# Performance work log

Hardware: AMD Instinct MI355X
Metric: run time of the kernel (lower is better)

Reference implementation:

```python
import jax, jax.numpy as jnp
import numpy as np

N_GRAPHS = 500
EPS = 1e-5


def setup_inputs() -> dict:
    key = jax.random.key(0)
    ks = jax.random.split(key, 10)
    N, H, OUT, E = 50000, 96, 10, 800000
    s = 1.0 / np.sqrt(H)
    x = jax.random.normal(ks[0], (N, H), jnp.float32)
    edge_index = jax.random.randint(ks[1], (2, E), 0, N, jnp.int32)
    batch = jnp.sort(jax.random.randint(ks[2], (N,), 0, N_GRAPHS, jnp.int32))
    convW = jax.random.normal(ks[3], (6, H, H), jnp.float32) * s
    convB = jnp.zeros((6, H), jnp.float32)
    bnG = jnp.ones((5, H), jnp.float32)
    bnB = jnp.zeros((5, H), jnp.float32)
    W1 = jax.random.normal(ks[4], (H, H), jnp.float32) * s
    b1 = jnp.zeros((H,), jnp.float32)
    g1 = jnp.ones((H,), jnp.float32)
    be1 = jnp.zeros((H,), jnp.float32)
    W2 = jax.random.normal(ks[5], (H, H), jnp.float32) * s
    b2 = jnp.zeros((H,), jnp.float32)
    W3 = jax.random.normal(ks[6], (H, OUT), jnp.float32) * s
    b3 = jnp.zeros((OUT,), jnp.float32)
    return dict(x=x, edge_index=edge_index, batch=batch, convW=convW, convB=convB,
                bnG=bnG, bnB=bnB, W1=W1, b1=b1, g1=g1, be1=be1, W2=W2, b2=b2, W3=W3, b3=b3)


def _batchnorm(h, g, b):
    # track_running_stats=False -> always use batch statistics (biased var)
    mu = h.mean(axis=0)
    v = jnp.mean((h - mu) ** 2, axis=0)
    return (h - mu) * jax.lax.rsqrt(v + EPS) * g + b


def reference(x, edge_index, batch, convW, convB, bnG, bnB, W1, b1, g1, be1, W2, b2, W3, b3):
    N = x.shape[0]
    src, dst = edge_index[0], edge_index[1]
    # GCN symmetric normalization with self-loops: A_hat = D^-1/2 (A+I) D^-1/2
    deg = jnp.zeros((N,), x.dtype).at[dst].add(1.0) + 1.0  # +1 for self loop
    dinv = jax.lax.rsqrt(deg)
    ew = dinv[src] * dinv[dst]            # [E] edge weights
    self_w = dinv * dinv                   # [N] self-loop weights (1/deg)

    def gcn_conv(h, W, b):
        h = h @ W
        agg = jnp.zeros_like(h).at[dst].add(ew[:, None] * h[src])
        return agg + self_w[:, None] * h + b

    # PyG BasicGNN: layers 0..4 -> conv+norm+relu+dropout; layer 5 -> conv only.
    # Dropout is identity in eval mode.
    for i in range(6):
        x = gcn_conv(x, convW[i], convB[i])
        if i < 5:
            x = jax.nn.relu(_batchnorm(x, bnG[i], bnB[i]))

    # global_mean_pool over `batch`
    cnt = jax.ops.segment_sum(jnp.ones((N,), x.dtype), batch, num_segments=N_GRAPHS)
    pooled = jax.ops.segment_sum(x, batch, num_segments=N_GRAPHS) / jnp.maximum(cnt, 1.0)[:, None]

    # prediction head: Linear -> BN -> ReLU -> (Dropout) -> Linear -> ReLU -> Linear
    h = jax.nn.relu(_batchnorm(pooled @ W1 + b1, g1, be1))
    h = jax.nn.relu(h @ W2 + b2)
    return h @ W3 + b3
```

## Files before the change

kernel.cpp:

```cpp
#include <hip/hip_runtime.h>
#include <hip/hip_fp16.h>

#define HF 96
#define C4 24
#define CH 12
#define NGRAPHS 500
#define EPS 1e-5f

__device__ __forceinline__ float4 h4tof4(uint2 u) {
    __half2 a = *(__half2*)&u.x;
    __half2 b = *(__half2*)&u.y;
    float2 fa = __half22float2(a);
    float2 fb = __half22float2(b);
    return make_float4(fa.x, fa.y, fb.x, fb.y);
}


__global__ void count_kernel(const int* __restrict__ dst, int E, int* __restrict__ cnt) {
    int stride = gridDim.x * blockDim.x;
    for (int i = blockIdx.x * blockDim.x + threadIdx.x; i < E; i += stride)
        atomicAdd(&cnt[dst[i]], 1);
}

__global__ void node_init_kernel(const int* __restrict__ cnt, int N,
                                 float* __restrict__ dinv, float* __restrict__ selfw) {
    int stride = gridDim.x * blockDim.x;
    for (int i = blockIdx.x * blockDim.x + threadIdx.x; i < N; i += stride) {
        float d = (float)(cnt[i] + 1);
        dinv[i] = 1.0f / sqrtf(d);
        selfw[i] = 1.0f / d;
    }
}

__global__ void scan1_kernel(const int* __restrict__ cnt, int N, int* __restrict__ bsum) {
    __shared__ int s[256];
    int t = threadIdx.x;
    int i = blockIdx.x * 256 + t;
    s[t] = (i < N) ? cnt[i] : 0;
    __syncthreads();
    for (int off = 128; off; off >>= 1) {
        if (t < off) s[t] += s[t + off];
        __syncthreads();
    }
    if (t == 0) bsum[blockIdx.x] = s[0];
}

__global__ void scan2_kernel(const int* __restrict__ bsum, int NB,
                             int* __restrict__ boff, int* __restrict__ row_ptr, int N) {
    __shared__ int s[256];
    int t = threadIdx.x;
    int v = (t < NB) ? bsum[t] : 0;
    s[t] = v;
    __syncthreads();
    for (int off = 1; off < 256; off <<= 1) {
        int u = (t >= off) ? s[t - off] : 0;
        __syncthreads();
        s[t] += u;
        __syncthreads();
    }
    if (t < NB) boff[t] = s[t] - v;
    if (t == 255) row_ptr[N] = s[255];
}

__global__ void scan3_kernel(int* __restrict__ cnt, int N, const int* __restrict__ boff,
                             int* __restrict__ row_ptr) {
    __shared__ int s[256];
    int t = threadIdx.x;
    int i = blockIdx.x * 256 + t;
    int v = (i < N) ? cnt[i] : 0;
    s[t] = v;
    __syncthreads();
    for (int off = 1; off < 256; off <<= 1) {
        int u = (t >= off) ? s[t - off] : 0;
        __syncthreads();
        s[t] += u;
        __syncthreads();
    }
    if (i < N) {
        row_ptr[i] = boff[blockIdx.x] + s[t] - v;
        cnt[i] = 0;
    }
}

__global__ void scatter_kernel(const int* __restrict__ src, const int* __restrict__ dst, int E,
                               const int* __restrict__ row_ptr, int* __restrict__ cnt,
                               const float* __restrict__ dinv,
                               int2* __restrict__ csr) {
    int stride = gridDim.x * blockDim.x;
    for (int i = blockIdx.x * blockDim.x + threadIdx.x; i < E; i += stride) {
        int d = dst[i], s = src[i];
        int p = row_ptr[d] + atomicAdd(&cnt[d], 1);
        float w = dinv[s] * dinv[d];
        csr[p] = make_int2(s, __float_as_int(w));
    }
}


__global__ __launch_bounds__(256) void
matmul_kernel(const float* __restrict__ in, const float* __restrict__ W,
              __half* __restrict__ out, int N, int applyBN,
              const double* __restrict__ bnsum,
              const float* __restrict__ bnG, const float* __restrict__ bnB) {
    __shared__ float4 sW[HF * C4];
    __shared__ float4 sAl[C4], sBe[C4];
    for (int i = threadIdx.x; i < HF * C4; i += blockDim.x)
        sW[i] = ((const float4*)W)[i];
    if (threadIdx.x < HF) {
        float a = 1.f, b = 0.f;
        if (applyBN) {
            double invN = 1.0 / (double)N;
            double mu = bnsum[threadIdx.x] * invN;
            double var = bnsum[HF + threadIdx.x] * invN - mu * mu;
            float v = fmaxf((float)var, 0.f) + EPS;
            a = bnG[threadIdx.x] / sqrtf(v);
            b = bnB[threadIdx.x] - (float)mu * a;
        }
        ((float*)sAl)[threadIdx.x] = a;
        ((float*)sBe)[threadIdx.x] = b;
    }
    __syncthreads();
    int nG = (N + 3) >> 2;
    int total = nG * C4;
    int stride = gridDim.x * blockDim.x;
    for (int idx = blockIdx.x * blockDim.x + threadIdx.x; idx < total; idx += stride) {
        int ng = idx / C4, c = idx % C4;
        int n0 = ng * 4;
        int rem = N - n0;
        const float4* r0 = (const float4*)(in + (size_t)n0 * HF);
        const float4* r1 = r0 + ((rem > 1) ? C4 : 0);
        const float4* r2 = r0 + ((rem > 2) ? 2 * C4 : 0);
        const float4* r3 = r0 + ((rem > 3) ? 3 * C4 : 0);
        float4 acc0 = make_float4(0.f, 0.f, 0.f, 0.f);
        float4 acc1 = acc0, acc2 = acc0, acc3 = acc0;
#pragma unroll 4
        for (int k4 = 0; k4 < C4; ++k4) {
            float4 al = sAl[k4], be = sBe[k4];
            float4 w0 = sW[(k4 * 4 + 0) * C4 + c];
            float4 w1 = sW[(k4 * 4 + 1) * C4 + c];
            float4 w2 = sW[(k4 * 4 + 2) * C4 + c];
            float4 w3 = sW[(k4 * 4 + 3) * C4 + c];
            float4 a0 = r0[k4], a1 = r1[k4], a2 = r2[k4], a3 = r3[k4];
            if (applyBN) {
                a0.x = fmaxf(fmaf(a0.x, al.x, be.x), 0.f); a0.y = fmaxf(fmaf(a0.y, al.y, be.y), 0.f);
                a0.z = fmaxf(fmaf(a0.z, al.z, be.z), 0.f); a0.w = fmaxf(fmaf(a0.w, al.w, be.w), 0.f);
                a1.x = fmaxf(fmaf(a1.x, al.x, be.x), 0.f); a1.y = fmaxf(fmaf(a1.y, al.y, be.y), 0.f);
                a1.z = fmaxf(fmaf(a1.z, al.z, be.z), 0.f); a1.w = fmaxf(fmaf(a1.w, al.w, be.w), 0.f);
                a2.x = fmaxf(fmaf(a2.x, al.x, be.x), 0.f); a2.y = fmaxf(fmaf(a2.y, al.y, be.y), 0.f);
                a2.z = fmaxf(fmaf(a2.z, al.z, be.z), 0.f); a2.w = fmaxf(fmaf(a2.w, al.w, be.w), 0.f);
                a3.x = fmaxf(fmaf(a3.x, al.x, be.x), 0.f); a3.y = fmaxf(fmaf(a3.y, al.y, be.y), 0.f);
                a3.z = fmaxf(fmaf(a3.z, al.z, be.z), 0.f); a3.w = fmaxf(fmaf(a3.w, al.w, be.w), 0.f);
            }
#define ACC(ACCV, AV) \
            ACCV.x = fmaf(AV.x, w0.x, fmaf(AV.y, w1.x, fmaf(AV.z, w2.x, fmaf(AV.w, w3.x, ACCV.x)))); \
            ACCV.y = fmaf(AV.x, w0.y, fmaf(AV.y, w1.y, fmaf(AV.z, w2.y, fmaf(AV.w, w3.y, ACCV.y)))); \
            ACCV.z = fmaf(AV.x, w0.z, fmaf(AV.y, w1.z, fmaf(AV.z, w2.z, fmaf(AV.w, w3.z, ACCV.z)))); \
            ACCV.w = fmaf(AV.x, w0.w, fmaf(AV.y, w1.w, fmaf(AV.z, w2.w, fmaf(AV.w, w3.w, ACCV.w))));
            ACC(acc0, a0) ACC(acc1, a1) ACC(acc2, a2) ACC(acc3, a3)
#undef ACC
        }
        uint2* orow = (uint2*)out;
#define STORE(J, ACCV) \
        if (rem > J) { \
            __half2 lo = __floats2half2_rn(ACCV.x, ACCV.y); \
            __half2 hi = __floats2half2_rn(ACCV.z, ACCV.w); \
            orow[(size_t)(n0 + J) * C4 + c] = make_uint2(*(unsigned int*)&lo, *(unsigned int*)&hi); \
        }
        STORE(0, acc0) STORE(1, acc1) STORE(2, acc2) STORE(3, acc3)
#undef STORE
    }
}


__global__ __launch_bounds__(256) void
agg_kernel(const __half* __restrict__ Hb, float* __restrict__ out,
           const int* __restrict__ row_ptr, const int2* __restrict__ csr,
           const float* __restrict__ selfw, const float* __restrict__ convB,
           int N, double* __restrict__ bnsum) {
    __shared__ float sred[2 * HF];
    bool stats = (bnsum != nullptr);
    for (int i = threadIdx.x; i < 2 * HF; i += blockDim.x) sred[i] = 0.f;
    __syncthreads();
    const uint4* h4p = (const uint4*)Hb;
    int total = N * CH;
    int stride = gridDim.x * blockDim.x;
    for (int idx = blockIdx.x * blockDim.x + threadIdx.x; idx < total; idx += stride) {
        int n = idx / CH, c = idx % CH;
        const uint4* hp = h4p + c;
        int p0 = row_ptr[n], p1 = row_ptr[n + 1];
        float sw = selfw[n];
        uint4 hraw = hp[(size_t)n * CH];
        float4 hlo = h4tof4(make_uint2(hraw.x, hraw.y));
        float4 hhi = h4tof4(make_uint2(hraw.z, hraw.w));
        float4 blo = ((const float4*)convB)[2 * c];
        float4 bhi = ((const float4*)convB)[2 * c + 1];
        float4 alo, ahi;
        alo.x = fmaf(sw, hlo.x, blo.x); alo.y = fmaf(sw, hlo.y, blo.y);
        alo.z = fmaf(sw, hlo.z, blo.z); alo.w = fmaf(sw, hlo.w, blo.w);
        ahi.x = fmaf(sw, hhi.x, bhi.x); ahi.y = fmaf(sw, hhi.y, bhi.y);
        ahi.z = fmaf(sw, hhi.z, bhi.z); ahi.w = fmaf(sw, hhi.w, bhi.w);
#define EDGE(EV, RV) { \
            float w = __int_as_float(EV.y); \
            float4 vlo = h4tof4(make_uint2(RV.x, RV.y)); \
            float4 vhi = h4tof4(make_uint2(RV.z, RV.w)); \
            alo.x = fmaf(w, vlo.x, alo.x); alo.y = fmaf(w, vlo.y, alo.y); \
            alo.z = fmaf(w, vlo.z, alo.z); alo.w = fmaf(w, vlo.w, alo.w); \
            ahi.x = fmaf(w, vhi.x, ahi.x); ahi.y = fmaf(w, vhi.y, ahi.y); \
            ahi.z = fmaf(w, vhi.z, ahi.z); ahi.w = fmaf(w, vhi.w, ahi.w); }
        int p = p0;
        for (; p + 8 <= p1; p += 8) {
            int2 e0 = csr[p + 0], e1 = csr[p + 1], e2 = csr[p + 2], e3 = csr[p + 3];
            int2 e4 = csr[p + 4], e5 = csr[p + 5], e6 = csr[p + 6], e7 = csr[p + 7];
            uint4 g0 = hp[(size_t)e0.x * CH];
            uint4 g1 = hp[(size_t)e1.x * CH];
            uint4 g2 = hp[(size_t)e2.x * CH];
            uint4 g3 = hp[(size_t)e3.x * CH];
            uint4 g4 = hp[(size_t)e4.x * CH];
            uint4 g5 = hp[(size_t)e5.x * CH];
            uint4 g6 = hp[(size_t)e6.x * CH];
            uint4 g7 = hp[(size_t)e7.x * CH];
            EDGE(e0, g0) EDGE(e1, g1) EDGE(e2, g2) EDGE(e3, g3)
            EDGE(e4, g4) EDGE(e5, g5) EDGE(e6, g6) EDGE(e7, g7)
        }
        for (; p + 4 <= p1; p += 4) {
            int2 e0 = csr[p + 0], e1 = csr[p + 1], e2 = csr[p + 2], e3 = csr[p + 3];
            uint4 g0 = hp[(size_t)e0.x * CH];
            uint4 g1 = hp[(size_t)e1.x * CH];
            uint4 g2 = hp[(size_t)e2.x * CH];
            uint4 g3 = hp[(size_t)e3.x * CH];
            EDGE(e0, g0) EDGE(e1, g1) EDGE(e2, g2) EDGE(e3, g3)
        }
        for (; p < p1; ++p) {
            int2 e = csr[p];
            uint4 g = hp[(size_t)e.x * CH];
            EDGE(e, g)
        }
#undef EDGE
        ((float4*)out)[2 * idx]     = alo;
        ((float4*)out)[2 * idx + 1] = ahi;
        if (stats) {
            int f = 8 * c;
            atomicAdd(&sred[f + 0], alo.x); atomicAdd(&sred[f + 1], alo.y);
            atomicAdd(&sred[f + 2], alo.z); atomicAdd(&sred[f + 3], alo.w);
            atomicAdd(&sred[f + 4], ahi.x); atomicAdd(&sred[f + 5], ahi.y);
            atomicAdd(&sred[f + 6], ahi.z); atomicAdd(&sred[f + 7], ahi.w);
            atomicAdd(&sred[HF + f + 0], alo.x * alo.x); atomicAdd(&sred[HF + f + 1], alo.y * alo.y);
            atomicAdd(&sred[HF + f + 2], alo.z * alo.z); atomicAdd(&sred[HF + f + 3], alo.w * alo.w);
            atomicAdd(&sred[HF + f + 4], ahi.x * ahi.x); atomicAdd(&sred[HF + f + 5], ahi.y * ahi.y);
            atomicAdd(&sred[HF + f + 6], ahi.z * ahi.z); atomicAdd(&sred[HF + f + 7], ahi.w * ahi.w);
        }
    }
    if (stats) {
        __syncthreads();
        for (int i = threadIdx.x; i < 2 * HF; i += blockDim.x)
            atomicAdd(&bnsum[i], (double)sred[i]);
    }
}


__global__ __launch_bounds__(128) void
pool_head1_kernel(const float* __restrict__ xin, const int* __restrict__ batch, int N,
                  const float* __restrict__ W1, const float* __restrict__ b1,
                  float* __restrict__ tmp1, double* __restrict__ bnsum) {
    __shared__ float row[HF];
    int g = blockIdx.x;
    int lo = 0, hi = N;
    while (lo < hi) { int m = (lo + hi) >> 1; if (batch[m] < g) lo = m + 1; else hi = m; }
    int s0 = lo;
    lo = s0; hi = N;
    while (lo < hi) { int m = (lo + hi) >> 1; if (batch[m] < g + 1) lo = m + 1; else hi = m; }
    int s1 = lo;
    int f = threadIdx.x;
    if (f < HF) {
        float sum = 0.f;
        for (int n = s0; n < s1; ++n) sum += xin[(size_t)n * HF + f];
        float inv = 1.0f / fmaxf((float)(s1 - s0), 1.0f);
        row[f] = sum * inv;
    }
    __syncthreads();
    if (f < HF) {
        float acc = b1[f];
        for (int k = 0; k < HF; ++k) acc = fmaf(row[k], W1[k * HF + f], acc);
        tmp1[g * HF + f] = acc;
        atomicAdd(&bnsum[f], (double)acc);
        atomicAdd(&bnsum[HF + f], (double)(acc * acc));
    }
}

__global__ __launch_bounds__(128) void
head23_kernel(const float* __restrict__ tmp1, const double* __restrict__ bnsum,
              const float* __restrict__ g1, const float* __restrict__ be1,
              const float* __restrict__ W2, const float* __restrict__ b2,
              const float* __restrict__ W3, const float* __restrict__ b3,
              float* __restrict__ out) {
    __shared__ float row[HF], row2[HF];
    int g = blockIdx.x;
    int f = threadIdx.x;
    if (f < HF) {
        double mu = bnsum[f] / (double)NGRAPHS;
        double var = bnsum[HF + f] / (double)NGRAPHS - mu * mu;
        float v = fmaxf((float)var, 0.f) + EPS;
        float a = g1[f] / sqrtf(v);
        float bb = be1[f] - (float)mu * a;
        row[f] = fmaxf(fmaf(tmp1[g * HF + f], a, bb), 0.f);
    }
    __syncthreads();
    if (f < HF) {
        float acc = b2[f];
        for (int k = 0; k < HF; ++k) acc = fmaf(row[k], W2[k * HF + f], acc);
        row2[f] = fmaxf(acc, 0.f);
    }
    __syncthreads();
    if (f < 10) {
        float acc = b3[f];
        for (int k = 0; k < HF; ++k) acc = fmaf(row2[k], W3[k * 10 + f], acc);
        out[g * 10 + f] = acc;
    }
}


extern "C" void kernel_launch(void* const* d_in, const int* in_sizes, int n_in,
                              void* d_out, int out_size, void* d_ws, size_t ws_size,
                              hipStream_t stream) {
    (void)n_in; (void)out_size; (void)ws_size;
    const float* x     = (const float*)d_in[0];
    const int*   ei    = (const int*)d_in[1];
    const int*   batch = (const int*)d_in[2];
    const float* convW = (const float*)d_in[3];
    const float* convB = (const float*)d_in[4];
    const float* bnG   = (const float*)d_in[5];
    const float* bnB   = (const float*)d_in[6];
    const float* W1    = (const float*)d_in[7];
    const float* b1    = (const float*)d_in[8];
    const float* g1    = (const float*)d_in[9];
    const float* be1   = (const float*)d_in[10];
    const float* W2    = (const float*)d_in[11];
    const float* b2    = (const float*)d_in[12];
    const float* W3    = (const float*)d_in[13];
    const float* b3    = (const float*)d_in[14];
    float* outp = (float*)d_out;

    int N = in_sizes[0] / HF;
    int E = in_sizes[1] / 2;
    int NB = (N + 255) / 256;
    const int* src  = ei;
    const int* dstp = ei + E;

    char* ws = (char*)d_ws;
    size_t off = 0;
    auto alloc = [&](size_t bytes) -> char* {
        char* p = ws + off;
        off += (bytes + 255) & ~(size_t)255;
        return p;
    };
    __half* Hb     = (__half*)alloc((size_t)N * HF * 2);
    float* Ob      = (float*)alloc((size_t)N * HF * 4);
    int2*  csr     = (int2*)alloc((size_t)E * 8);
    int*   row_ptr = (int*)alloc((size_t)(N + 1) * 4);
    float* dinv    = (float*)alloc((size_t)N * 4);
    float* selfw   = (float*)alloc((size_t)N * 4);
    int*   bsum    = (int*)alloc((size_t)NB * 4);
    int*   boff    = (int*)alloc((size_t)NB * 4);
    float* tmp1    = (float*)alloc((size_t)NGRAPHS * HF * 4);
    char* zstart   = ws + off;
    int*    cnt    = (int*)alloc((size_t)N * 4);
    double* bns    = (double*)alloc(6 * 2 * HF * 8);
    size_t zbytes  = (size_t)((ws + off) - zstart);

    hipMemsetAsync(zstart, 0, zbytes, stream);

    count_kernel<<<1024, 256, 0, stream>>>(dstp, E, cnt);
    node_init_kernel<<<(N + 255) / 256, 256, 0, stream>>>(cnt, N, dinv, selfw);
    scan1_kernel<<<NB, 256, 0, stream>>>(cnt, N, bsum);
    scan2_kernel<<<1, 256, 0, stream>>>(bsum, NB, boff, row_ptr, N);
    scan3_kernel<<<NB, 256, 0, stream>>>(cnt, N, boff, row_ptr);
    scatter_kernel<<<1024, 256, 0, stream>>>(src, dstp, E, row_ptr, cnt, dinv, csr);

    int agg_grid = (N * CH + 255) / 256;
    const float* cur = x;
    for (int i = 0; i < 6; ++i) {
        int nG = (N + 3) >> 2;
        int mm_grid = (nG * C4 + 255) / 256;
        matmul_kernel<<<mm_grid, 256, 0, stream>>>(
            cur, convW + (size_t)i * HF * HF, Hb, N,
            (i > 0) ? 1 : 0,
            (i > 0) ? bns + (size_t)(i - 1) * 2 * HF : nullptr,
            (i > 0) ? bnG + (size_t)(i - 1) * HF : nullptr,
            (i > 0) ? bnB + (size_t)(i - 1) * HF : nullptr);
        agg_kernel<<<agg_grid, 256, 0, stream>>>(
            Hb, Ob, row_ptr, csr, selfw,
            convB + (size_t)i * HF, N,
            (i < 5) ? bns + (size_t)i * 2 * HF : nullptr);
        cur = Ob;
    }

    pool_head1_kernel<<<NGRAPHS, 128, 0, stream>>>(Ob, batch, N, W1, b1, tmp1, bns + 5 * 2 * HF);
    head23_kernel<<<NGRAPHS, 128, 0, stream>>>(tmp1, bns + 5 * 2 * HF, g1, be1, W2, b2, W3, b3, outp);
}
```

Baseline: 854.1 us.

## Use MFMA fp16 matmul, parallelize mean pooling, shrink aggregation unroll

Replaces the scalar fp32 FMA node-feature matmul with a tiled kernel. It stages 64 BN+ReLU-transformed input rows and a transposed weight tile in shared memory as fp16, then uses 16x16x32 MFMA instructions. Global mean pooling is split into a separate kernel in which many threads each sum a slice of a graph's nodes with float4 loads and combine partials with atomics; the old version had one block per graph summing serially. The edge-aggregation loop also drops its 8-way unrolled body and keeps only the 4-way one. In exchange, inputs are rounded to fp16 before the matmul, and the atomic accumulation makes pooled sums order-nondeterministic.

```diff
diff --git a/kernel.cpp b/kernel.cpp
--- a/kernel.cpp
+++ b/kernel.cpp
@@ -5,7 +5,13 @@
 #define C4 24
 #define CH 12
 #define NGRAPHS 500
+#define POOL_SL 8
+#define MMROWS 64
+#define ATP 104
 #define EPS 1e-5f
+
+typedef _Float16 half8 __attribute__((ext_vector_type(8)));
+typedef float f32x4 __attribute__((ext_vector_type(4)));
 
 __device__ __forceinline__ float4 h4tof4(uint2 u) {
     __half2 a = *(__half2*)&u.x;
@@ -98,75 +104,83 @@
 
 __global__ __launch_bounds__(256) void
 matmul_kernel(const float* __restrict__ in, const float* __restrict__ W,
-              __half* __restrict__ out, int N, int applyBN,
+              _Float16* __restrict__ out, int N, int applyBN,
               const double* __restrict__ bnsum,
               const float* __restrict__ bnG, const float* __restrict__ bnB) {
-    __shared__ float4 sW[HF * C4];
-    __shared__ float4 sAl[C4], sBe[C4];
-    for (int i = threadIdx.x; i < HF * C4; i += blockDim.x)
-        sW[i] = ((const float4*)W)[i];
-    if (threadIdx.x < HF) {
+    __shared__ _Float16 At[MMROWS][ATP];
+    __shared__ _Float16 Wt[HF][ATP];
+    __shared__ float sAl[HF], sBe[HF];
+    int t = threadIdx.x;
+    int n0 = blockIdx.x * MMROWS;
+    int rows = N - n0; if (rows > MMROWS) rows = MMROWS;
+
+    if (t < HF) {
         float a = 1.f, b = 0.f;
         if (applyBN) {
             double invN = 1.0 / (double)N;
-            double mu = bnsum[threadIdx.x] * invN;
-            double var = bnsum[HF + threadIdx.x] * invN - mu * mu;
+            double mu = bnsum[t] * invN;
+            double var = bnsum[HF + t] * invN - mu * mu;
             float v = fmaxf((float)var, 0.f) + EPS;
-            a = bnG[threadIdx.x] / sqrtf(v);
-            b = bnB[threadIdx.x] - (float)mu * a;
-        }
-        ((float*)sAl)[threadIdx.x] = a;
-        ((float*)sBe)[threadIdx.x] = b;
-    }
-    __syncthreads();
-    int nG = (N + 3) >> 2;
-    int total = nG * C4;
-    int stride = gridDim.x * blockDim.x;
-    for (int idx = blockIdx.x * blockDim.x + threadIdx.x; idx < total; idx += stride) {
-        int ng = idx / C4, c = idx % C4;
-        int n0 = ng * 4;
-        int rem = N - n0;
-        const float4* r0 = (const float4*)(in + (size_t)n0 * HF);
-        const float4* r1 = r0 + ((rem > 1) ? C4 : 0);
-        const float4* r2 = r0 + ((rem > 2) ? 2 * C4 : 0);
-        const float4* r3 = r0 + ((rem > 3) ? 3 * C4 : 0);
-        float4 acc0 = make_float4(0.f, 0.f, 0.f, 0.f);
-        float4 acc1 = acc0, acc2 = acc0, acc3 = acc0;
-#pragma unroll 4
-        for (int k4 = 0; k4 < C4; ++k4) {
-            float4 al = sAl[k4], be = sBe[k4];
-            float4 w0 = sW[(k4 * 4 + 0) * C4 + c];
-            float4 w1 = sW[(k4 * 4 + 1) * C4 + c];
-            float4 w2 = sW[(k4 * 4 + 2) * C4 + c];
-            float4 w3 = sW[(k4 * 4 + 3) * C4 + c];
-            float4 a0 = r0[k4], a1 = r1[k4], a2 = r2[k4], a3 = r3[k4];
+            a = bnG[t] / sqrtf(v);
+            b = bnB[t] - (float)mu * a;
+        }
+        sAl[t] = a; sBe[t] = b;
+    }
+    __syncthreads();
+
+#pragma unroll
+    for (int j = 0; j < 6; ++j) {
+        int gi = t + j * 256;
+        int r = gi / C4, c4 = gi % C4;
+        if (r < rows) {
+            float4 v = ((const float4*)(in + (size_t)(n0 + r) * HF))[c4];
+            int k = c4 * 4;
             if (applyBN) {
-                a0.x = fmaxf(fmaf(a0.x, al.x, be.x), 0.f); a0.y = fmaxf(fmaf(a0.y, al.y, be.y), 0.f);
-                a0.z = fmaxf(fmaf(a0.z, al.z, be.z), 0.f); a0.w = fmaxf(fmaf(a0.w, al.w, be.w), 0.f);
-                a1.x = fmaxf(fmaf(a1.x, al.x, be.x), 0.f); a1.y = fmaxf(fmaf(a1.y, al.y, be.y), 0.f);
-                a1.z = fmaxf(fmaf(a1.z, al.z, be.z), 0.f); a1.w = fmaxf(fmaf(a1.w, al.w, be.w), 0.f);
-                a2.x = fmaxf(fmaf(a2.x, al.x, be.x), 0.f); a2.y = fmaxf(fmaf(a2.y, al.y, be.y), 0.f);
-                a2.z = fmaxf(fmaf(a2.z, al.z, be.z), 0.f); a2.w = fmaxf(fmaf(a2.w, al.w, be.w), 0.f);
-                a3.x = fmaxf(fmaf(a3.x, al.x, be.x), 0.f); a3.y = fmaxf(fmaf(a3.y, al.y, be.y), 0.f);
-                a3.z = fmaxf(fmaf(a3.z, al.z, be.z), 0.f); a3.w = fmaxf(fmaf(a3.w, al.w, be.w), 0.f);
+                v.x = fmaxf(fmaf(v.x, sAl[k + 0], sBe[k + 0]), 0.f);
+                v.y = fmaxf(fmaf(v.y, sAl[k + 1], sBe[k + 1]), 0.f);
+                v.z = fmaxf(fmaf(v.z, sAl[k + 2], sBe[k + 2]), 0.f);
+                v.w = fmaxf(fmaf(v.w, sAl[k + 3], sBe[k + 3]), 0.f);
             }
-#define ACC(ACCV, AV) \
-            ACCV.x = fmaf(AV.x, w0.x, fmaf(AV.y, w1.x, fmaf(AV.z, w2.x, fmaf(AV.w, w3.x, ACCV.x)))); \
-            ACCV.y = fmaf(AV.x, w0.y, fmaf(AV.y, w1.y, fmaf(AV.z, w2.y, fmaf(AV.w, w3.y, ACCV.y)))); \
-            ACCV.z = fmaf(AV.x, w0.z, fmaf(AV.y, w1.z, fmaf(AV.z, w2.z, fmaf(AV.w, w3.z, ACCV.z)))); \
-            ACCV.w = fmaf(AV.x, w0.w, fmaf(AV.y, w1.w, fmaf(AV.z, w2.w, fmaf(AV.w, w3.w, ACCV.w))));
-            ACC(acc0, a0) ACC(acc1, a1) ACC(acc2, a2) ACC(acc3, a3)
-#undef ACC
-        }
-        uint2* orow = (uint2*)out;
-#define STORE(J, ACCV) \
-        if (rem > J) { \
-            __half2 lo = __floats2half2_rn(ACCV.x, ACCV.y); \
-            __half2 hi = __floats2half2_rn(ACCV.z, ACCV.w); \
-            orow[(size_t)(n0 + J) * C4 + c] = make_uint2(*(unsigned int*)&lo, *(unsigned int*)&hi); \
-        }
-        STORE(0, acc0) STORE(1, acc1) STORE(2, acc2) STORE(3, acc3)
-#undef STORE
+            At[r][k + 0] = (_Float16)v.x; At[r][k + 1] = (_Float16)v.y;
+            At[r][k + 2] = (_Float16)v.z; At[r][k + 3] = (_Float16)v.w;
+        }
+    }
+#pragma unroll
+    for (int j = 0; j < 9; ++j) {
+        int gi = t + j * 256;
+        int k = gi / C4, f4 = gi % C4;
+        float4 v = ((const float4*)(W + (size_t)k * HF))[f4];
+        int f = f4 * 4;
+        Wt[f + 0][k] = (_Float16)v.x; Wt[f + 1][k] = (_Float16)v.y;
+        Wt[f + 2][k] = (_Float16)v.z; Wt[f + 3][k] = (_Float16)v.w;
+    }
+    __syncthreads();
+
+    int w = t >> 6;
+    int lane = t & 63;
+    int arow = w * 16 + (lane & 15);
+    int k0 = (lane >> 4) * 8;
+    f32x4 acc[6];
+#pragma unroll
+    for (int ft = 0; ft < 6; ++ft) acc[ft] = (f32x4){0.f, 0.f, 0.f, 0.f};
+#pragma unroll
+    for (int ks = 0; ks < 3; ++ks) {
+        half8 a = *(const half8*)&At[arow][ks * 32 + k0];
+#pragma unroll
+        for (int ft = 0; ft < 6; ++ft) {
+            half8 b = *(const half8*)&Wt[ft * 16 + (lane & 15)][ks * 32 + k0];
+            acc[ft] = __builtin_amdgcn_mfma_f32_16x16x32_f16(a, b, acc[ft], 0, 0, 0);
+        }
+    }
+    int fcol = lane & 15;
+#pragma unroll
+    for (int ft = 0; ft < 6; ++ft) {
+#pragma unroll
+        for (int j = 0; j < 4; ++j) {
+            int r = w * 16 + (lane >> 4) * 4 + j;
+            if (r < rows)
+                out[(size_t)(n0 + r) * HF + ft * 16 + fcol] = (_Float16)acc[ft][j];
+        }
     }
 }
 
@@ -207,22 +221,8 @@
             ahi.x = fmaf(w, vhi.x, ahi.x); ahi.y = fmaf(w, vhi.y, ahi.y); \
             ahi.z = fmaf(w, vhi.z, ahi.z); ahi.w = fmaf(w, vhi.w, ahi.w); }
         int p = p0;
-        for (; p + 8 <= p1; p += 8) {
-            int2 e0 = csr[p + 0], e1 = csr[p + 1], e2 = csr[p + 2], e3 = csr[p + 3];
-            int2 e4 = csr[p + 4], e5 = csr[p + 5], e6 = csr[p + 6], e7 = csr[p + 7];
-            uint4 g0 = hp[(size_t)e0.x * CH];
-            uint4 g1 = hp[(size_t)e1.x * CH];
-            uint4 g2 = hp[(size_t)e2.x * CH];
-            uint4 g3 = hp[(size_t)e3.x * CH];
-            uint4 g4 = hp[(size_t)e4.x * CH];
-            uint4 g5 = hp[(size_t)e5.x * CH];
-            uint4 g6 = hp[(size_t)e6.x * CH];
-            uint4 g7 = hp[(size_t)e7.x * CH];
-            EDGE(e0, g0) EDGE(e1, g1) EDGE(e2, g2) EDGE(e3, g3)
-            EDGE(e4, g4) EDGE(e5, g5) EDGE(e6, g6) EDGE(e7, g7)
-        }
         for (; p + 4 <= p1; p += 4) {
-            int2 e0 = csr[p + 0], e1 = csr[p + 1], e2 = csr[p + 2], e3 = csr[p + 3];
+            int2 e0 = csr[p], e1 = csr[p + 1], e2 = csr[p + 2], e3 = csr[p + 3];
             uint4 g0 = hp[(size_t)e0.x * CH];
             uint4 g1 = hp[(size_t)e1.x * CH];
             uint4 g2 = hp[(size_t)e2.x * CH];
@@ -257,10 +257,39 @@
 }
 
 
+__global__ __launch_bounds__(256) void
+pool_kernel(const float* __restrict__ xin, const int* __restrict__ batch, int N,
+            float* __restrict__ pooled) {
+    int idx = blockIdx.x * blockDim.x + threadIdx.x;
+    int total = NGRAPHS * POOL_SL * C4;
+    if (idx >= total) return;
+    int c = idx % C4;
+    int q = (idx / C4) % POOL_SL;
+    int g = idx / (C4 * POOL_SL);
+    int lo = 0, hi = N;
+    while (lo < hi) { int m = (lo + hi) >> 1; if (batch[m] < g) lo = m + 1; else hi = m; }
+    int s0 = lo;
+    lo = s0; hi = N;
+    while (lo < hi) { int m = (lo + hi) >> 1; if (batch[m] < g + 1) lo = m + 1; else hi = m; }
+    int len = lo - s0;
+    int n0 = s0 + (len * q) / POOL_SL;
+    int n1 = s0 + (len * (q + 1)) / POOL_SL;
+    const float4* x4 = (const float4*)xin;
+    float4 acc = make_float4(0.f, 0.f, 0.f, 0.f);
+    for (int n = n0; n < n1; ++n) {
+        float4 v0 = x4[(size_t)n * C4 + c];
+        acc.x += v0.x; acc.y += v0.y; acc.z += v0.z; acc.w += v0.w;
+    }
+    atomicAdd(&pooled[g * HF + 4 * c + 0], acc.x);
+    atomicAdd(&pooled[g * HF + 4 * c + 1], acc.y);
+    atomicAdd(&pooled[g * HF + 4 * c + 2], acc.z);
+    atomicAdd(&pooled[g * HF + 4 * c + 3], acc.w);
+}
+
 __global__ __launch_bounds__(128) void
-pool_head1_kernel(const float* __restrict__ xin, const int* __restrict__ batch, int N,
-                  const float* __restrict__ W1, const float* __restrict__ b1,
-                  float* __restrict__ tmp1, double* __restrict__ bnsum) {
+head1_kernel(const float* __restrict__ pooled, const int* __restrict__ batch, int N,
+             const float* __restrict__ W1, const float* __restrict__ b1,
+             float* __restrict__ tmp1, double* __restrict__ bnsum) {
     __shared__ float row[HF];
     int g = blockIdx.x;
     int lo = 0, hi = N;
@@ -268,14 +297,10 @@
     int s0 = lo;
     lo = s0; hi = N;
     while (lo < hi) { int m = (lo + hi) >> 1; if (batch[m] < g + 1) lo = m + 1; else hi = m; }
-    int s1 = lo;
+    int len = lo - s0;
+    float inv = 1.0f / fmaxf((float)len, 1.0f);
     int f = threadIdx.x;
-    if (f < HF) {
-        float sum = 0.f;
-        for (int n = s0; n < s1; ++n) sum += xin[(size_t)n * HF + f];
-        float inv = 1.0f / fmaxf((float)(s1 - s0), 1.0f);
-        row[f] = sum * inv;
-    }
+    if (f < HF) row[f] = pooled[g * HF + f] * inv;
     __syncthreads();
     if (f < HF) {
         float acc = b1[f];
@@ -352,7 +377,7 @@
         off += (bytes + 255) & ~(size_t)255;
         return p;
     };
-    __half* Hb     = (__half*)alloc((size_t)N * HF * 2);
+    _Float16* Hb   = (_Float16*)alloc((size_t)N * HF * 2);
     float* Ob      = (float*)alloc((size_t)N * HF * 4);
     int2*  csr     = (int2*)alloc((size_t)E * 8);
     int*   row_ptr = (int*)alloc((size_t)(N + 1) * 4);
@@ -364,6 +389,7 @@
     char* zstart   = ws + off;
     int*    cnt    = (int*)alloc((size_t)N * 4);
     double* bns    = (double*)alloc(6 * 2 * HF * 8);
+    float*  pooled = (float*)alloc((size_t)NGRAPHS * HF * 4);
     size_t zbytes  = (size_t)((ws + off) - zstart);
 
     hipMemsetAsync(zstart, 0, zbytes, stream);
@@ -376,10 +402,9 @@
     scatter_kernel<<<1024, 256, 0, stream>>>(src, dstp, E, row_ptr, cnt, dinv, csr);
 
     int agg_grid = (N * CH + 255) / 256;
+    int mm_grid = (N + MMROWS - 1) / MMROWS;
     const float* cur = x;
     for (int i = 0; i < 6; ++i) {
-        int nG = (N + 3) >> 2;
-        int mm_grid = (nG * C4 + 255) / 256;
         matmul_kernel<<<mm_grid, 256, 0, stream>>>(
             cur, convW + (size_t)i * HF * HF, Hb, N,
             (i > 0) ? 1 : 0,
@@ -387,12 +412,14 @@
             (i > 0) ? bnG + (size_t)(i - 1) * HF : nullptr,
             (i > 0) ? bnB + (size_t)(i - 1) * HF : nullptr);
         agg_kernel<<<agg_grid, 256, 0, stream>>>(
-            Hb, Ob, row_ptr, csr, selfw,
+            (const __half*)Hb, Ob, row_ptr, csr, selfw,
             convB + (size_t)i * HF, N,
             (i < 5) ? bns + (size_t)i * 2 * HF : nullptr);
         cur = Ob;
     }
 
-    pool_head1_kernel<<<NGRAPHS, 128, 0, stream>>>(Ob, batch, N, W1, b1, tmp1, bns + 5 * 2 * HF);
+    int pool_grid = (NGRAPHS * POOL_SL * C4 + 255) / 256;
+    pool_kernel<<<pool_grid, 256, 0, stream>>>(Ob, batch, N, pooled);
+    head1_kernel<<<NGRAPHS, 128, 0, stream>>>(pooled, batch, N, W1, b1, tmp1, bns + 5 * 2 * HF);
     head23_kernel<<<NGRAPHS, 128, 0, stream>>>(tmp1, bns + 5 * 2 * HF, g1, be1, W2, b2, W3, b3, outp);
 }
```

New measurement: 750.5 us. -12.1%, faster.
